# Kernel tuning notes

Hardware: AMD Instinct MI355X
Metric: run time of the kernel (lower is better)

Reference implementation:

```python
import jax, jax.numpy as jnp
import numpy as np

S = 2048   # sample_batch
N = 16     # num_h (agents per sample group)
OBS = 8
PRED = 12
H = 16     # hidden / embed size


def _lstm_cell(x, h, c, Wi, Wh, b):
    # torch LSTMCell gate order: i, f, g, o
    g = x @ Wi + h @ Wh + b
    i, f, gg, o = jnp.split(g, 4, axis=-1)
    c = jax.nn.sigmoid(f) * c + jax.nn.sigmoid(i) * jnp.tanh(gg)
    h = jax.nn.sigmoid(o) * jnp.tanh(c)
    return h, c


def setup_inputs() -> dict:
    key = jax.random.key(0)
    ks = jax.random.split(key, 16)
    B = S * N
    p = lambda k, sh: jax.random.normal(k, sh, jnp.float32) * 0.1
    return dict(
        traj_rel=jax.random.normal(ks[0], (OBS, B, 2), jnp.float32),
        obs_traj_pos=jax.random.normal(ks[1], (OBS, B, 2), jnp.float32),
        nei_index=jax.random.randint(ks[2], (B, N), 0, 2, jnp.int32),
        noise=jax.random.normal(ks[3], (PRED, B, 2), jnp.float32),
        enc_emb_W=p(ks[4], (2, H)), enc_emb_b=jnp.zeros((H,), jnp.float32),
        enc_Wi=p(ks[5], (H, 4 * H)), enc_Wh=p(ks[6], (H, 4 * H)), enc_b=jnp.zeros((4 * H,), jnp.float32),
        dec_in_W=p(ks[7], (H + 2, H)), dec_in_b=jnp.zeros((H,), jnp.float32),
        dec_Wi=p(ks[8], (H, 4 * H)), dec_Wh=p(ks[9], (H, 4 * H)), dec_b=jnp.zeros((4 * H,), jnp.float32),
        pool_rel_W=p(ks[10], (2, H)), pool_rel_b=jnp.zeros((H,), jnp.float32),
        pool_mlp_W=p(ks[11], (2 * H, H)), pool_mlp_b=jnp.zeros((H,), jnp.float32),
        out_W=p(ks[12], (H, 4)), out_b=jnp.zeros((4,), jnp.float32),
    )


def reference(traj_rel, obs_traj_pos, nei_index, noise,
              enc_emb_W, enc_emb_b, enc_Wi, enc_Wh, enc_b,
              dec_in_W, dec_in_b, dec_Wi, dec_Wh, dec_b,
              pool_rel_W, pool_rel_b, pool_mlp_W, pool_mlp_b,
              out_W, out_b):
    B = traj_rel.shape[1]
    mask = nei_index > 0  # (B, N)

    # --- history encoder: embed + LSTM over obs steps, take last hidden ---
    def enc_step(carry, x):
        h, c = carry
        e = jax.nn.relu(x @ enc_emb_W + enc_emb_b)
        h, c = _lstm_cell(e, h, c, enc_Wi, enc_Wh, enc_b)
        return (h, c), None

    h0 = jnp.zeros((B, H), traj_rel.dtype)
    (h_enc, _), _ = jax.lax.scan(enc_step, (h0, h0), traj_rel[:OBS])

    # --- neighbor pooling: embed relative pos, concat neighbor hidden, MLP, masked max-pool ---
    def pool(rel, h):
        re = jax.nn.relu(rel @ pool_rel_W + pool_rel_b)  # (B, N, H)
        hn = jnp.broadcast_to(h.reshape(S, 1, N, H), (S, N, N, H)).reshape(B, N, H)
        feat = jax.nn.relu(jnp.concatenate([re, hn], -1) @ pool_mlp_W + pool_mlp_b)
        masked = jnp.where(mask[..., None], feat, -1e9)
        pooled = masked.max(axis=1)  # (B, H)
        has = mask.any(axis=1, keepdims=True)
        return jnp.where(has, pooled, 0.0)

    def dec_step(carry, noise_t):
        h, c, ctx, out, pos = carry
        inp = jax.lax.stop_gradient(jnp.concatenate([ctx, out], -1))  # .detach() in torch
        e = jax.nn.relu(inp @ dec_in_W + dec_in_b)
        h, c = _lstm_cell(e, h, c, dec_Wi, dec_Wh, dec_b)
        p = pos.reshape(S, N, 2)
        # rel[s,i,j] = pos[s,i] - pos[s,j]  (matches expand/transpose subtraction)
        rel = (p[:, :, None, :] - p[:, None, :, :]).reshape(B, N, 2)
        ctx = pool(rel, h)
        o4 = (h + ctx) @ out_W + out_b
        mu = o4[:, :2]
        scale = jnp.clip(o4[:, 2:], -9.0, 4.0)
        std = jnp.exp(scale)
        pred = mu + std * noise_t
        pos = jax.lax.stop_gradient(pos + pred)
        return (h, c, ctx, pred, pos), (pred, mu, std)

    init = (h_enc, jnp.zeros_like(h_enc), jnp.zeros_like(h_enc),
            traj_rel[OBS - 1], obs_traj_pos[-1])
    _, (pred, mu, std) = jax.lax.scan(dec_step, init, noise)
    return pred, mu, std  # each (PRED, B, 2)
```

## Files before the change

kernel.cpp:

```cpp
#include <hip/hip_runtime.h>

#define S_    2048
#define N_    16
#define OBS_  8
#define PRED_ 12
#define B_    (S_*N_)
#define SCN_  2

typedef __attribute__((ext_vector_type(8))) short short8;
typedef __attribute__((ext_vector_type(4))) float floatx4;
typedef __attribute__((ext_vector_type(4))) unsigned uintx4;
typedef unsigned short ushort_t;

__device__ __forceinline__ float sigmf(float x) { return __builtin_amdgcn_rcpf(1.0f + __expf(-x)); }
__device__ __forceinline__ float tanhx(float x) { return fmaf(-2.0f, __builtin_amdgcn_rcpf(1.0f + __expf(2.0f*x)), 1.0f); }
__device__ __forceinline__ unsigned bfhi(float f) {
  return __builtin_bit_cast(unsigned, f) + 0x8000u;
}
__device__ __forceinline__ unsigned pack2bf(float lo, float hi) {
  return __builtin_amdgcn_perm(bfhi(hi), bfhi(lo), 0x07060302);
}
__device__ __forceinline__ ushort_t f2bf1(float f) { return (ushort_t)(bfhi(f) >> 16); }
__device__ __forceinline__ float rlanef(float v, int lane) {
  return __builtin_bit_cast(float, __builtin_amdgcn_readlane(__builtin_bit_cast(int, v), lane));
}
__device__ __forceinline__ unsigned shflu(unsigned v, int src) {
  return (unsigned)__shfl((int)v, src, 64);
}
__device__ __forceinline__ unsigned shflxu(unsigned v, int m) {
  return (unsigned)__shfl_xor((int)v, m, 64);
}

extern "C" __global__ __launch_bounds__(128, 2) void traj_ar_kernel(
    const float* __restrict__ traj_rel, const float* __restrict__ obs_pos,
    const int*  __restrict__ nei,       const float* __restrict__ noise,
    const float* __restrict__ eeW, const float* __restrict__ eeb,
    const float* __restrict__ eWi, const float* __restrict__ eWh, const float* __restrict__ eb,
    const float* __restrict__ diW, const float* __restrict__ dib,
    const float* __restrict__ dWi, const float* __restrict__ dWh, const float* __restrict__ db,
    const float* __restrict__ prW, const float* __restrict__ prb,
    const float* __restrict__ mW,  const float* __restrict__ mb,
    const float* __restrict__ oW,  const float* __restrict__ ob,
    float* __restrict__ out)
{
  __shared__ __align__(16) float h_s[SCN_][256];
  __shared__ __align__(16) float ctx_s[SCN_][256];
  __shared__ __align__(16) ushort_t ctx_bf[SCN_][384];
  __shared__            unsigned sm_s[SCN_][16];

  const int tid = threadIdx.x;
  const int w  = tid >> 6;
  const int l  = tid & 63;
  const int lq = l >> 4;
  const int lc = l & 15;
  const int u0 = lq*4;
  const int s  = blockIdx.x*SCN_ + w;
  const bool hi_half = (lq >= 2);
  const int esrc0 = (lq & 1)*32 + lc;
  const int esrc1 = esrc0 + 16;

  {
    unsigned* cz = (unsigned*)ctx_bf[w];
    cz[l] = 0; cz[64+l] = 0; cz[128+l] = 0;
  }
  float POSX = obs_pos[((OBS_-1)*B_ + s*N_ + lc)*2 + 0];
  float POSY = obs_pos[((OBS_-1)*B_ + s*N_ + lc)*2 + 1];
  unsigned prevu;
  {
    float pvx = traj_rel[((OBS_-1)*B_ + s*N_ + lc)*2 + 0];
    float pvy = traj_rel[((OBS_-1)*B_ + s*N_ + lc)*2 + 1];
    prevu = pack2bf(pvx, pvy);
  }
  {
    const int a = l >> 2, nb = (l & 3)*4;
    const int4 nv = *(const int4*)&nei[(s*N_ + a)*N_ + nb];
    unsigned bits = 0;
    bits |= (nv.x > 0) ? (1u << (nb+0)) : 0u;
    bits |= (nv.y > 0) ? (1u << (nb+1)) : 0u;
    bits |= (nv.z > 0) ? (1u << (nb+2)) : 0u;
    bits |= (nv.w > 0) ? (1u << (nb+3)) : 0u;
    bits |= __shfl_xor(bits, 1, 64);
    bits |= __shfl_xor(bits, 2, 64);
    if ((l & 3) == 0) sm_s[w][a] = bits;
  }

  short8 bfrag;
  {
    uintx4 bw;
    #pragma unroll
    for (int p = 0; p < 4; ++p)
      bw[p] = pack2bf(mW[(8*lq + 2*p)*16 + lc], mW[(8*lq + 2*p + 1)*16 + lc]);
    bfrag = __builtin_bit_cast(short8, bw);
  }
  const float bm = mb[lc];

  float pWx[8], pWy[8], pB[8];
  {
    const int wu0 = (lq & 1) * 8;
    #pragma unroll
    for (int j = 0; j < 8; ++j) {
      pWx[j] = prW[wu0 + j];
      pWy[j] = prW[16 + wu0 + j];
      pB[j]  = prb[wu0 + j];
    }
  }

  float oWc[16];
  #pragma unroll
  for (int m = 0; m < 16; ++m) oWc[m] = oW[m*4 + lq];
  const float obia = ob[lq];

  float ew0[4], ew1[4], ebv[4];
  #pragma unroll
  for (int r = 0; r < 4; ++r) {
    ew0[r] = eeW[u0+r]; ew1[r] = eeW[16+u0+r]; ebv[r] = eeb[u0+r];
  }

  const int row0 = (lq & 1) * 8;

  #define LOAD_GATE_FRAG(A, C, Wi_, Wh_, bias_, g) {                                      \
    const float* gsrc_ = (lq & 2) ? (Wh_) : (Wi_);                                        \
    uintx4 aw_;                                                                           \
    aw_[0] = pack2bf(gsrc_[(row0+0)*64 + (g)*16 + lc], gsrc_[(row0+1)*64 + (g)*16 + lc]); \
    aw_[1] = pack2bf(gsrc_[(row0+2)*64 + (g)*16 + lc], gsrc_[(row0+3)*64 + (g)*16 + lc]); \
    aw_[2] = pack2bf(gsrc_[(row0+4)*64 + (g)*16 + lc], gsrc_[(row0+5)*64 + (g)*16 + lc]); \
    aw_[3] = pack2bf(gsrc_[(row0+6)*64 + (g)*16 + lc], gsrc_[(row0+7)*64 + (g)*16 + lc]); \
    (A) = __builtin_bit_cast(short8, aw_);                                                \
    (C)[0] = (bias_)[(g)*16 + u0 + 0]; (C)[1] = (bias_)[(g)*16 + u0 + 1];                 \
    (C)[2] = (bias_)[(g)*16 + u0 + 2]; (C)[3] = (bias_)[(g)*16 + u0 + 3];                 \
  }

  short8 eA0, eA1, eA2, eA3; floatx4 eC0, eC1, eC2, eC3;
  LOAD_GATE_FRAG(eA0, eC0, eWi, eWh, eb, 0);
  LOAD_GATE_FRAG(eA1, eC1, eWi, eWh, eb, 1);
  LOAD_GATE_FRAG(eA2, eC2, eWi, eWh, eb, 2);
  LOAD_GATE_FRAG(eA3, eC3, eWi, eWh, eb, 3);

  #define LSTM_EW(r, hv) {                                                            \
    float ig = sigmf(dI[r]), fg = sigmf(dF[r]), gv = tanhx(dG[r]), og = sigmf(dO[r]); \
    c4[r] = fg*c4[r] + ig*gv;                                                         \
    hv = og * tanhx(c4[r]);                                                           \
  }

  uintx4 hf; hf[0]=0; hf[1]=0; hf[2]=0; hf[3]=0;

  floatx4 c4 = {0.0f, 0.0f, 0.0f, 0.0f};
  const float2* xr2 = (const float2*)traj_rel;
  for (int t = 0; t < OBS_; ++t) {
    float2 x = xr2[t*B_ + s*N_ + lc];
    float e0 = fmaxf(fmaf(x.y, ew1[0], fmaf(x.x, ew0[0], ebv[0])), 0.0f);
    float e1 = fmaxf(fmaf(x.y, ew1[1], fmaf(x.x, ew0[1], ebv[1])), 0.0f);
    float e2 = fmaxf(fmaf(x.y, ew1[2], fmaf(x.x, ew0[2], ebv[2])), 0.0f);
    float e3 = fmaxf(fmaf(x.y, ew1[3], fmaf(x.x, ew0[3], ebv[3])), 0.0f);
    uint2 ep; ep.x = pack2bf(e0, e1); ep.y = pack2bf(e2, e3);
    uintx4 eu;
    eu[0] = shflu(ep.x, esrc0); eu[1] = shflu(ep.y, esrc0);
    eu[2] = shflu(ep.x, esrc1); eu[3] = shflu(ep.y, esrc1);
    uintx4 bu = (lq < 2) ? eu : hf;
    short8 bfr = __builtin_bit_cast(short8, bu);
    floatx4 dI = __builtin_amdgcn_mfma_f32_16x16x32_bf16(eA0, bfr, eC0, 0, 0, 0);
    floatx4 dF = __builtin_amdgcn_mfma_f32_16x16x32_bf16(eA1, bfr, eC1, 0, 0, 0);
    floatx4 dG = __builtin_amdgcn_mfma_f32_16x16x32_bf16(eA2, bfr, eC2, 0, 0, 0);
    floatx4 dO = __builtin_amdgcn_mfma_f32_16x16x32_bf16(eA3, bfr, eC3, 0, 0, 0);
    float h40, h41, h42, h43;
    LSTM_EW(0, h40); LSTM_EW(1, h41); LSTM_EW(2, h42); LSTM_EW(3, h43);
    uint2 hp2; hp2.x = pack2bf(h40, h41); hp2.y = pack2bf(h42, h43);
    hf[0] = shflu(hp2.x, esrc0); hf[1] = shflu(hp2.y, esrc0);
    hf[2] = shflu(hp2.x, esrc1); hf[3] = shflu(hp2.y, esrc1);
  }

  short8 dA0, dA1, dA2, dA3; floatx4 dC0, dC1, dC2, dC3;
  LOAD_GATE_FRAG(dA0, dC0, dWi, dWh, db, 0);
  LOAD_GATE_FRAG(dA1, dC1, dWi, dWh, db, 1);
  LOAD_GATE_FRAG(dA2, dC2, dWi, dWh, db, 2);
  LOAD_GATE_FRAG(dA3, dC3, dWi, dWh, db, 3);

  short8 diA; floatx4 diC;
  {
    uintx4 aw; aw[0]=0; aw[1]=0; aw[2]=0; aw[3]=0;
    if (lq < 2) {
      const int r0 = lq*8;
      #pragma unroll
      for (int p = 0; p < 4; ++p)
        aw[p] = pack2bf(diW[(r0+2*p)*16 + lc], diW[(r0+2*p+1)*16 + lc]);
    } else if (lq == 2) {
      aw[0] = pack2bf(diW[16*16 + lc], diW[17*16 + lc]);
    }
    diA = __builtin_bit_cast(short8, aw);
    #pragma unroll
    for (int r = 0; r < 4; ++r) diC[r] = dib[u0 + r];
  }

  floatx4 cm[16];
  #pragma unroll
  for (int tt = 0; tt < 16; ++tt) {
    const unsigned mi = sm_s[w][tt];
    #pragma unroll
    for (int r = 0; r < 4; ++r)
      cm[tt][r] = ((mi >> (u0 + r)) & 1u) ? bm : -1e9f;
  }

  #define MK_REFRAG(pp, F0, F1) {                                           \
    const int t0_ = 2*(pp), t1_ = 2*(pp)+1;                                 \
    float rx0_ = PXs[t0_] - POSX, ry0_ = PYs[t0_] - POSY;                   \
    float rx1_ = PXs[t1_] - POSX, ry1_ = PYs[t1_] - POSY;                   \
    float rx_ = hi_half ? rx1_ : rx0_;                                      \
    float ry_ = hi_half ? ry1_ : ry0_;                                      \
    float rr_[8];                                                           \
    _Pragma("unroll")                                                       \
    for (int j = 0; j < 8; ++j)                                             \
      rr_[j] = fmaxf(fmaf(ry_, pWy[j], fmaf(rx_, pWx[j], pB[j])), 0.0f);    \
    (F0)[0] = pack2bf(rr_[0], rr_[1]);                                      \
    (F0)[1] = pack2bf(rr_[2], rr_[3]);                                      \
    (F0)[2] = pack2bf(rr_[4], rr_[5]);                                      \
    (F0)[3] = pack2bf(rr_[6], rr_[7]);                                      \
    (F1)[0] = shflxu((F0)[0], 32);                                          \
    (F1)[1] = shflxu((F0)[1], 32);                                          \
    (F1)[2] = shflxu((F0)[2], 32);                                          \
    (F1)[3] = shflxu((F0)[3], 32);                                          \
  }

  #define POOL_TILE(tt, FRAG) {                                             \
    short8 a_ = hi_half ? __builtin_bit_cast(short8, hf)                    \
                        : __builtin_bit_cast(short8, FRAG);                 \
    floatx4 d_ = __builtin_amdgcn_mfma_f32_16x16x32_bf16(a_, bfrag, cm[tt], 0, 0, 0); \
    float pm_ = fmaxf(fmaxf(d_[0], d_[1]), fmaxf(d_[2], d_[3]));            \
    pm_ = fmaxf(pm_, __shfl_xor(pm_, 16, 64));                              \
    pm_ = fmaxf(pm_, __shfl_xor(pm_, 32, 64));                              \
    if (lq == ((tt) & 3)) {                                                 \
      float cvv_ = fmaxf(pm_, 0.0f);                                        \
      ctx_s[w][(tt)*16 + lc] = cvv_;                                        \
      ctx_bf[w][(tt)*24 + lc] = f2bf1(cvv_);                                \
    }                                                                       \
  }

  c4 = (floatx4){0.0f, 0.0f, 0.0f, 0.0f};
  const int MU_OFF = PRED_*B_*2;
  const int SD_OFF = 2*PRED_*B_*2;
  for (int t = 0; t < PRED_; ++t) {
    const float nz = noise[(t*B_ + s*N_ + lc)*2 + (lq&1)];
    float PXs[16], PYs[16];
    #pragma unroll
    for (int a2 = 0; a2 < 16; ++a2) {
      PXs[a2] = rlanef(POSX, a2);
      PYs[a2] = rlanef(POSY, a2);
    }
    uintx4 g0, g1;
    MK_REFRAG(0, g0, g1);
    uint2 ep;
    {
      short8 cv = *(const short8*)&ctx_bf[w][lc*24 + (lq&1)*8];
      uintx4 pz; pz[0] = prevu; pz[1]=0; pz[2]=0; pz[3]=0;
      short8 pv = __builtin_bit_cast(short8, pz);
      short8 zz = {0,0,0,0,0,0,0,0};
      short8 bf1 = (lq < 2) ? cv : ((lq == 2) ? pv : zz);
      floatx4 d = __builtin_amdgcn_mfma_f32_16x16x32_bf16(diA, bf1, diC, 0, 0, 0);
      ep.x = pack2bf(fmaxf(d[0],0.0f), fmaxf(d[1],0.0f));
      ep.y = pack2bf(fmaxf(d[2],0.0f), fmaxf(d[3],0.0f));
    }
    {
      uintx4 eu;
      eu[0] = shflu(ep.x, esrc0); eu[1] = shflu(ep.y, esrc0);
      eu[2] = shflu(ep.x, esrc1); eu[3] = shflu(ep.y, esrc1);
      uintx4 bu = (lq < 2) ? eu : hf;
      short8 bfr = __builtin_bit_cast(short8, bu);
      floatx4 dI = __builtin_amdgcn_mfma_f32_16x16x32_bf16(dA0, bfr, dC0, 0, 0, 0);
      floatx4 dF = __builtin_amdgcn_mfma_f32_16x16x32_bf16(dA1, bfr, dC1, 0, 0, 0);
      floatx4 dG = __builtin_amdgcn_mfma_f32_16x16x32_bf16(dA2, bfr, dC2, 0, 0, 0);
      floatx4 dO = __builtin_amdgcn_mfma_f32_16x16x32_bf16(dA3, bfr, dC3, 0, 0, 0);
      float h40, h41, h42, h43;
      LSTM_EW(0, h40); LSTM_EW(1, h41); LSTM_EW(2, h42); LSTM_EW(3, h43);
      uint2 hp2; hp2.x = pack2bf(h40, h41); hp2.y = pack2bf(h42, h43);
      hf[0] = shflu(hp2.x, esrc0); hf[1] = shflu(hp2.y, esrc0);
      hf[2] = shflu(hp2.x, esrc1); hf[3] = shflu(hp2.y, esrc1);
      floatx4 hv4; hv4[0]=h40; hv4[1]=h41; hv4[2]=h42; hv4[3]=h43;
      *(floatx4*)&h_s[w][lc*16 + u0] = hv4;
    }
    {
      #pragma unroll
      for (int p = 0; p < 8; ++p) {
        uintx4 n0, n1;
        if (p < 7) MK_REFRAG(p+1, n0, n1);
        POOL_TILE(2*p,     g0);
        POOL_TILE(2*p + 1, g1);
        g0 = n0; g1 = n1;
      }
    }
    {
      float acc = obia;
      const floatx4* hp4 = (const floatx4*)&h_s[w][lc*16];
      const floatx4* cx4 = (const floatx4*)&ctx_s[w][lc*16];
      #pragma unroll
      for (int mm = 0; mm < 4; ++mm) {
        floatx4 hv = hp4[mm];
        floatx4 cv = cx4[mm];
        #pragma unroll
        for (int r = 0; r < 4; ++r)
          acc = fmaf(hv[r]+cv[r], oWc[mm*4+r], acc);
      }
      float sc = __shfl_down(acc, 32, 64);
      float mu = acc;
      float scale = fminf(fmaxf(sc, -9.0f), 4.0f);
      float sd = __expf(scale);
      float pr = fmaf(sd, nz, mu);
      if (lq < 2) {
        int o = (t*B_ + s*N_ + lc)*2 + lq;
        out[o]          = pr;
        out[MU_OFF + o] = mu;
        out[SD_OFF + o] = sd;
      }
      float prx = __shfl(pr, lc, 64);
      float pry = __shfl(pr, 16 + lc, 64);
      POSX += prx;
      POSY += pry;
      prevu = pack2bf(prx, pry);
    }
  }
  #undef LSTM_EW
  #undef LOAD_GATE_FRAG
  #undef MK_REFRAG
  #undef POOL_TILE
}

extern "C" void kernel_launch(void* const* d_in, const int* in_sizes, int n_in,
                              void* d_out, int out_size, void* d_ws, size_t ws_size,
                              hipStream_t stream) {
  (void)in_sizes; (void)n_in; (void)d_ws; (void)ws_size; (void)out_size;
  traj_ar_kernel<<<dim3(S_/SCN_), dim3(128), 0, stream>>>(
      (const float*)d_in[0],  (const float*)d_in[1],  (const int*)d_in[2],   (const float*)d_in[3],
      (const float*)d_in[4],  (const float*)d_in[5],  (const float*)d_in[6], (const float*)d_in[7],
      (const float*)d_in[8],  (const float*)d_in[9],  (const float*)d_in[10],(const float*)d_in[11],
      (const float*)d_in[12], (const float*)d_in[13], (const float*)d_in[14],(const float*)d_in[15],
      (const float*)d_in[16], (const float*)d_in[17], (const float*)d_in[18],(const float*)d_in[19],
      (float*)d_out);
}
```

Measured before the change: 160.7 us.

## Process two sample groups per wavefront with interleaved independent chains

Each wavefront now handles two sample groups (A and B) instead of one. Every phase of the encoder, decoder LSTM, pooling and output is duplicated and interleaved so that two independent dependency chains can hide MFMA and transcendental latency within a single wave. This doubles per-thread register state (two mask arrays, positions and fragments), and the launch bound drops to a minimum of 1 block per CU, which risks lower occupancy or spills. The grid halves to S/4 blocks of 128 threads.

Result: slower. 197.7 us (+23.1%).

```diff
diff --git a/kernel.cpp b/kernel.cpp
--- a/kernel.cpp
+++ b/kernel.cpp
@@ -5,7 +5,7 @@
 #define OBS_  8
 #define PRED_ 12
 #define B_    (S_*N_)
-#define SCN_  2
+#define SCN_  4
 
 typedef __attribute__((ext_vector_type(8))) short short8;
 typedef __attribute__((ext_vector_type(4))) float floatx4;
@@ -31,7 +31,7 @@
   return (unsigned)__shfl_xor((int)v, m, 64);
 }
 
-extern "C" __global__ __launch_bounds__(128, 2) void traj_ar_kernel(
+extern "C" __global__ __launch_bounds__(128, 1) void traj_ar_kernel(
     const float* __restrict__ traj_rel, const float* __restrict__ obs_pos,
     const int*  __restrict__ nei,       const float* __restrict__ noise,
     const float* __restrict__ eeW, const float* __restrict__ eeb,
@@ -54,35 +54,45 @@
   const int lq = l >> 4;
   const int lc = l & 15;
   const int u0 = lq*4;
-  const int s  = blockIdx.x*SCN_ + w;
   const bool hi_half = (lq >= 2);
+  const int slA = w*2, slB = w*2 + 1;
+  const int sA = blockIdx.x*SCN_ + slA;
+  const int sB = sA + 1;
   const int esrc0 = (lq & 1)*32 + lc;
   const int esrc1 = esrc0 + 16;
 
-  {
-    unsigned* cz = (unsigned*)ctx_bf[w];
-    cz[l] = 0; cz[64+l] = 0; cz[128+l] = 0;
-  }
-  float POSX = obs_pos[((OBS_-1)*B_ + s*N_ + lc)*2 + 0];
-  float POSY = obs_pos[((OBS_-1)*B_ + s*N_ + lc)*2 + 1];
-  unsigned prevu;
-  {
-    float pvx = traj_rel[((OBS_-1)*B_ + s*N_ + lc)*2 + 0];
-    float pvy = traj_rel[((OBS_-1)*B_ + s*N_ + lc)*2 + 1];
-    prevu = pack2bf(pvx, pvy);
-  }
-  {
-    const int a = l >> 2, nb = (l & 3)*4;
-    const int4 nv = *(const int4*)&nei[(s*N_ + a)*N_ + nb];
-    unsigned bits = 0;
-    bits |= (nv.x > 0) ? (1u << (nb+0)) : 0u;
-    bits |= (nv.y > 0) ? (1u << (nb+1)) : 0u;
-    bits |= (nv.z > 0) ? (1u << (nb+2)) : 0u;
-    bits |= (nv.w > 0) ? (1u << (nb+3)) : 0u;
-    bits |= __shfl_xor(bits, 1, 64);
-    bits |= __shfl_xor(bits, 2, 64);
-    if ((l & 3) == 0) sm_s[w][a] = bits;
-  }
+  { unsigned* cz = (unsigned*)ctx_bf[slA]; cz[l]=0; cz[64+l]=0; cz[128+l]=0; }
+  { unsigned* cz = (unsigned*)ctx_bf[slB]; cz[l]=0; cz[64+l]=0; cz[128+l]=0; }
+
+  float POSXA = obs_pos[((OBS_-1)*B_ + sA*N_ + lc)*2 + 0];
+  float POSYA = obs_pos[((OBS_-1)*B_ + sA*N_ + lc)*2 + 1];
+  float POSXB = obs_pos[((OBS_-1)*B_ + sB*N_ + lc)*2 + 0];
+  float POSYB = obs_pos[((OBS_-1)*B_ + sB*N_ + lc)*2 + 1];
+  unsigned prevuA, prevuB;
+  {
+    float px = traj_rel[((OBS_-1)*B_ + sA*N_ + lc)*2 + 0];
+    float py = traj_rel[((OBS_-1)*B_ + sA*N_ + lc)*2 + 1];
+    prevuA = pack2bf(px, py);
+  }
+  {
+    float px = traj_rel[((OBS_-1)*B_ + sB*N_ + lc)*2 + 0];
+    float py = traj_rel[((OBS_-1)*B_ + sB*N_ + lc)*2 + 1];
+    prevuB = pack2bf(px, py);
+  }
+  #define MK_MASK(sS, slS) {                                                \
+    const int a_ = l >> 2, nb_ = (l & 3)*4;                                 \
+    const int4 nv_ = *(const int4*)&nei[((sS)*N_ + a_)*N_ + nb_];           \
+    unsigned bits_ = 0;                                                     \
+    bits_ |= (nv_.x > 0) ? (1u << (nb_+0)) : 0u;                            \
+    bits_ |= (nv_.y > 0) ? (1u << (nb_+1)) : 0u;                            \
+    bits_ |= (nv_.z > 0) ? (1u << (nb_+2)) : 0u;                            \
+    bits_ |= (nv_.w > 0) ? (1u << (nb_+3)) : 0u;                            \
+    bits_ |= __shfl_xor(bits_, 1, 64);                                      \
+    bits_ |= __shfl_xor(bits_, 2, 64);                                      \
+    if ((l & 3) == 0) sm_s[slS][a_] = bits_;                                \
+  }
+  MK_MASK(sA, slA)
+  MK_MASK(sB, slB)
 
   short8 bfrag;
   {
@@ -136,37 +146,44 @@
   LOAD_GATE_FRAG(eA2, eC2, eWi, eWh, eb, 2);
   LOAD_GATE_FRAG(eA3, eC3, eWi, eWh, eb, 3);
 
-  #define LSTM_EW(r, hv) {                                                            \
+  #define LSTM_EW(C4, r, hv) {                                                        \
     float ig = sigmf(dI[r]), fg = sigmf(dF[r]), gv = tanhx(dG[r]), og = sigmf(dO[r]); \
-    c4[r] = fg*c4[r] + ig*gv;                                                         \
-    hv = og * tanhx(c4[r]);                                                           \
-  }
-
-  uintx4 hf; hf[0]=0; hf[1]=0; hf[2]=0; hf[3]=0;
-
-  floatx4 c4 = {0.0f, 0.0f, 0.0f, 0.0f};
+    (C4)[r] = fg*(C4)[r] + ig*gv;                                                     \
+    hv = og * tanhx((C4)[r]);                                                         \
+  }
+
+  #define ENC_STEP(sS, C4, HF) {                                            \
+    float2 x_ = xr2[t*B_ + (sS)*N_ + lc];                                   \
+    float e0_ = fmaxf(fmaf(x_.y, ew1[0], fmaf(x_.x, ew0[0], ebv[0])), 0.0f);\
+    float e1_ = fmaxf(fmaf(x_.y, ew1[1], fmaf(x_.x, ew0[1], ebv[1])), 0.0f);\
+    float e2_ = fmaxf(fmaf(x_.y, ew1[2], fmaf(x_.x, ew0[2], ebv[2])), 0.0f);\
+    float e3_ = fmaxf(fmaf(x_.y, ew1[3], fmaf(x_.x, ew0[3], ebv[3])), 0.0f);\
+    uint2 ep_; ep_.x = pack2bf(e0_, e1_); ep_.y = pack2bf(e2_, e3_);        \
+    uintx4 eu_;                                                             \
+    eu_[0] = shflu(ep_.x, esrc0); eu_[1] = shflu(ep_.y, esrc0);             \
+    eu_[2] = shflu(ep_.x, esrc1); eu_[3] = shflu(ep_.y, esrc1);             \
+    uintx4 bu_ = (lq < 2) ? eu_ : (HF);                                     \
+    short8 bfr_ = __builtin_bit_cast(short8, bu_);                          \
+    floatx4 dI = __builtin_amdgcn_mfma_f32_16x16x32_bf16(eA0, bfr_, eC0, 0, 0, 0); \
+    floatx4 dF = __builtin_amdgcn_mfma_f32_16x16x32_bf16(eA1, bfr_, eC1, 0, 0, 0); \
+    floatx4 dG = __builtin_amdgcn_mfma_f32_16x16x32_bf16(eA2, bfr_, eC2, 0, 0, 0); \
+    floatx4 dO = __builtin_amdgcn_mfma_f32_16x16x32_bf16(eA3, bfr_, eC3, 0, 0, 0); \
+    float h40_, h41_, h42_, h43_;                                           \
+    LSTM_EW(C4, 0, h40_); LSTM_EW(C4, 1, h41_);                             \
+    LSTM_EW(C4, 2, h42_); LSTM_EW(C4, 3, h43_);                             \
+    uint2 hp2_; hp2_.x = pack2bf(h40_, h41_); hp2_.y = pack2bf(h42_, h43_); \
+    (HF)[0] = shflu(hp2_.x, esrc0); (HF)[1] = shflu(hp2_.y, esrc0);         \
+    (HF)[2] = shflu(hp2_.x, esrc1); (HF)[3] = shflu(hp2_.y, esrc1);         \
+  }
+
+  uintx4 hfA; hfA[0]=0; hfA[1]=0; hfA[2]=0; hfA[3]=0;
+  uintx4 hfB; hfB[0]=0; hfB[1]=0; hfB[2]=0; hfB[3]=0;
+
+  floatx4 c4A = {0.0f,0.0f,0.0f,0.0f}, c4B = {0.0f,0.0f,0.0f,0.0f};
   const float2* xr2 = (const float2*)traj_rel;
   for (int t = 0; t < OBS_; ++t) {
-    float2 x = xr2[t*B_ + s*N_ + lc];
-    float e0 = fmaxf(fmaf(x.y, ew1[0], fmaf(x.x, ew0[0], ebv[0])), 0.0f);
-    float e1 = fmaxf(fmaf(x.y, ew1[1], fmaf(x.x, ew0[1], ebv[1])), 0.0f);
-    float e2 = fmaxf(fmaf(x.y, ew1[2], fmaf(x.x, ew0[2], ebv[2])), 0.0f);
-    float e3 = fmaxf(fmaf(x.y, ew1[3], fmaf(x.x, ew0[3], ebv[3])), 0.0f);
-    uint2 ep; ep.x = pack2bf(e0, e1); ep.y = pack2bf(e2, e3);
-    uintx4 eu;
-    eu[0] = shflu(ep.x, esrc0); eu[1] = shflu(ep.y, esrc0);
-    eu[2] = shflu(ep.x, esrc1); eu[3] = shflu(ep.y, esrc1);
-    uintx4 bu = (lq < 2) ? eu : hf;
-    short8 bfr = __builtin_bit_cast(short8, bu);
-    floatx4 dI = __builtin_amdgcn_mfma_f32_16x16x32_bf16(eA0, bfr, eC0, 0, 0, 0);
-    floatx4 dF = __builtin_amdgcn_mfma_f32_16x16x32_bf16(eA1, bfr, eC1, 0, 0, 0);
-    floatx4 dG = __builtin_amdgcn_mfma_f32_16x16x32_bf16(eA2, bfr, eC2, 0, 0, 0);
-    floatx4 dO = __builtin_amdgcn_mfma_f32_16x16x32_bf16(eA3, bfr, eC3, 0, 0, 0);
-    float h40, h41, h42, h43;
-    LSTM_EW(0, h40); LSTM_EW(1, h41); LSTM_EW(2, h42); LSTM_EW(3, h43);
-    uint2 hp2; hp2.x = pack2bf(h40, h41); hp2.y = pack2bf(h42, h43);
-    hf[0] = shflu(hp2.x, esrc0); hf[1] = shflu(hp2.y, esrc0);
-    hf[2] = shflu(hp2.x, esrc1); hf[3] = shflu(hp2.y, esrc1);
+    ENC_STEP(sA, c4A, hfA)
+    ENC_STEP(sB, c4B, hfB)
   }
 
   short8 dA0, dA1, dA2, dA3; floatx4 dC0, dC1, dC2, dC3;
@@ -191,25 +208,28 @@
     for (int r = 0; r < 4; ++r) diC[r] = dib[u0 + r];
   }
 
-  floatx4 cm[16];
+  floatx4 cmA[16], cmB[16];
   #pragma unroll
   for (int tt = 0; tt < 16; ++tt) {
-    const unsigned mi = sm_s[w][tt];
-    #pragma unroll
-    for (int r = 0; r < 4; ++r)
-      cm[tt][r] = ((mi >> (u0 + r)) & 1u) ? bm : -1e9f;
-  }
-
-  #define MK_REFRAG(pp, F0, F1) {                                           \
+    const unsigned miA = sm_s[slA][tt];
+    const unsigned miB = sm_s[slB][tt];
+    #pragma unroll
+    for (int r = 0; r < 4; ++r) {
+      cmA[tt][r] = ((miA >> (u0 + r)) & 1u) ? bm : -1e9f;
+      cmB[tt][r] = ((miB >> (u0 + r)) & 1u) ? bm : -1e9f;
+    }
+  }
+
+  #define MK_REFRAG(PXs, PYs, pp, PX, PY, F0, F1) {                         \
     const int t0_ = 2*(pp), t1_ = 2*(pp)+1;                                 \
-    float rx0_ = PXs[t0_] - POSX, ry0_ = PYs[t0_] - POSY;                   \
-    float rx1_ = PXs[t1_] - POSX, ry1_ = PYs[t1_] - POSY;                   \
+    float rx0_ = (PXs)[t0_] - (PX), ry0_ = (PYs)[t0_] - (PY);               \
+    float rx1_ = (PXs)[t1_] - (PX), ry1_ = (PYs)[t1_] - (PY);               \
     float rx_ = hi_half ? rx1_ : rx0_;                                      \
     float ry_ = hi_half ? ry1_ : ry0_;                                      \
     float rr_[8];                                                           \
     _Pragma("unroll")                                                       \
-    for (int j = 0; j < 8; ++j)                                             \
-      rr_[j] = fmaxf(fmaf(ry_, pWy[j], fmaf(rx_, pWx[j], pB[j])), 0.0f);    \
+    for (int j_ = 0; j_ < 8; ++j_)                                          \
+      rr_[j_] = fmaxf(fmaf(ry_, pWy[j_], fmaf(rx_, pWx[j_], pB[j_])), 0.0f);\
     (F0)[0] = pack2bf(rr_[0], rr_[1]);                                      \
     (F0)[1] = pack2bf(rr_[2], rr_[3]);                                      \
     (F0)[2] = pack2bf(rr_[4], rr_[5]);                                      \
@@ -220,106 +240,127 @@
     (F1)[3] = shflxu((F0)[3], 32);                                          \
   }
 
-  #define POOL_TILE(tt, FRAG) {                                             \
-    short8 a_ = hi_half ? __builtin_bit_cast(short8, hf)                    \
+  #define POOL_TILE(slS, CM, tt, FRAG, HF) {                                \
+    short8 a_ = hi_half ? __builtin_bit_cast(short8, HF)                    \
                         : __builtin_bit_cast(short8, FRAG);                 \
-    floatx4 d_ = __builtin_amdgcn_mfma_f32_16x16x32_bf16(a_, bfrag, cm[tt], 0, 0, 0); \
+    floatx4 d_ = __builtin_amdgcn_mfma_f32_16x16x32_bf16(a_, bfrag, (CM)[tt], 0, 0, 0); \
     float pm_ = fmaxf(fmaxf(d_[0], d_[1]), fmaxf(d_[2], d_[3]));            \
     pm_ = fmaxf(pm_, __shfl_xor(pm_, 16, 64));                              \
     pm_ = fmaxf(pm_, __shfl_xor(pm_, 32, 64));                              \
     if (lq == ((tt) & 3)) {                                                 \
       float cvv_ = fmaxf(pm_, 0.0f);                                        \
-      ctx_s[w][(tt)*16 + lc] = cvv_;                                        \
-      ctx_bf[w][(tt)*24 + lc] = f2bf1(cvv_);                                \
+      ctx_s[slS][(tt)*16 + lc] = cvv_;                                      \
+      ctx_bf[slS][(tt)*24 + lc] = f2bf1(cvv_);                              \
     }                                                                       \
   }
 
-  c4 = (floatx4){0.0f, 0.0f, 0.0f, 0.0f};
+  #define PH1(slS, PREVU, EP) {                                             \
+    short8 cv_ = *(const short8*)&ctx_bf[slS][lc*24 + (lq&1)*8];            \
+    uintx4 pz_; pz_[0] = (PREVU); pz_[1]=0; pz_[2]=0; pz_[3]=0;             \
+    short8 pv_ = __builtin_bit_cast(short8, pz_);                           \
+    short8 zz_ = {0,0,0,0,0,0,0,0};                                         \
+    short8 bf1_ = (lq < 2) ? cv_ : ((lq == 2) ? pv_ : zz_);                 \
+    floatx4 d_ = __builtin_amdgcn_mfma_f32_16x16x32_bf16(diA, bf1_, diC, 0, 0, 0); \
+    (EP).x = pack2bf(fmaxf(d_[0],0.0f), fmaxf(d_[1],0.0f));                 \
+    (EP).y = pack2bf(fmaxf(d_[2],0.0f), fmaxf(d_[3],0.0f));                 \
+  }
+
+  #define PH2(slS, EP, C4, HF) {                                            \
+    uintx4 eu_;                                                             \
+    eu_[0] = shflu((EP).x, esrc0); eu_[1] = shflu((EP).y, esrc0);           \
+    eu_[2] = shflu((EP).x, esrc1); eu_[3] = shflu((EP).y, esrc1);           \
+    uintx4 bu_ = (lq < 2) ? eu_ : (HF);                                     \
+    short8 bfr_ = __builtin_bit_cast(short8, bu_);                          \
+    floatx4 dI = __builtin_amdgcn_mfma_f32_16x16x32_bf16(dA0, bfr_, dC0, 0, 0, 0); \
+    floatx4 dF = __builtin_amdgcn_mfma_f32_16x16x32_bf16(dA1, bfr_, dC1, 0, 0, 0); \
+    floatx4 dG = __builtin_amdgcn_mfma_f32_16x16x32_bf16(dA2, bfr_, dC2, 0, 0, 0); \
+    floatx4 dO = __builtin_amdgcn_mfma_f32_16x16x32_bf16(dA3, bfr_, dC3, 0, 0, 0); \
+    float h40_, h41_, h42_, h43_;                                           \
+    LSTM_EW(C4, 0, h40_); LSTM_EW(C4, 1, h41_);                             \
+    LSTM_EW(C4, 2, h42_); LSTM_EW(C4, 3, h43_);                             \
+    uint2 hp2_; hp2_.x = pack2bf(h40_, h41_); hp2_.y = pack2bf(h42_, h43_); \
+    (HF)[0] = shflu(hp2_.x, esrc0); (HF)[1] = shflu(hp2_.y, esrc0);         \
+    (HF)[2] = shflu(hp2_.x, esrc1); (HF)[3] = shflu(hp2_.y, esrc1);         \
+    floatx4 hv4_; hv4_[0]=h40_; hv4_[1]=h41_; hv4_[2]=h42_; hv4_[3]=h43_;   \
+    *(floatx4*)&h_s[slS][lc*16 + u0] = hv4_;                                \
+  }
+
+  #define PH5(slS, sS, NZ, PX, PY, PREVU) {                                 \
+    float acc_ = obia;                                                      \
+    const floatx4* hp4_ = (const floatx4*)&h_s[slS][lc*16];                 \
+    const floatx4* cx4_ = (const floatx4*)&ctx_s[slS][lc*16];               \
+    _Pragma("unroll")                                                       \
+    for (int mm_ = 0; mm_ < 4; ++mm_) {                                     \
+      floatx4 hv_ = hp4_[mm_];                                              \
+      floatx4 cv_ = cx4_[mm_];                                              \
+      _Pragma("unroll")                                                     \
+      for (int r_ = 0; r_ < 4; ++r_)                                        \
+        acc_ = fmaf(hv_[r_]+cv_[r_], oWc[mm_*4+r_], acc_);                  \
+    }                                                                       \
+    float sc_ = __shfl_down(acc_, 32, 64);                                  \
+    float mu_ = acc_;                                                       \
+    float scale_ = fminf(fmaxf(sc_, -9.0f), 4.0f);                          \
+    float sd_ = __expf(scale_);                                             \
+    float pr_ = fmaf(sd_, (NZ), mu_);                                       \
+    if (lq < 2) {                                                           \
+      int o_ = (t*B_ + (sS)*N_ + lc)*2 + lq;                                \
+      out[o_]          = pr_;                                               \
+      out[MU_OFF + o_] = mu_;                                               \
+      out[SD_OFF + o_] = sd_;                                               \
+    }                                                                       \
+    float prx_ = __shfl(pr_, lc, 64);                                       \
+    float pry_ = __shfl(pr_, 16 + lc, 64);                                  \
+    (PX) += prx_;                                                           \
+    (PY) += pry_;                                                           \
+    (PREVU) = pack2bf(prx_, pry_);                                          \
+  }
+
+  c4A = (floatx4){0.0f,0.0f,0.0f,0.0f};
+  c4B = (floatx4){0.0f,0.0f,0.0f,0.0f};
   const int MU_OFF = PRED_*B_*2;
   const int SD_OFF = 2*PRED_*B_*2;
   for (int t = 0; t < PRED_; ++t) {
-    const float nz = noise[(t*B_ + s*N_ + lc)*2 + (lq&1)];
-    float PXs[16], PYs[16];
+    const float nzA = noise[(t*B_ + sA*N_ + lc)*2 + (lq&1)];
+    const float nzB = noise[(t*B_ + sB*N_ + lc)*2 + (lq&1)];
+    float PXsA[16], PYsA[16], PXsB[16], PYsB[16];
     #pragma unroll
     for (int a2 = 0; a2 < 16; ++a2) {
-      PXs[a2] = rlanef(POSX, a2);
-      PYs[a2] = rlanef(POSY, a2);
-    }
-    uintx4 g0, g1;
-    MK_REFRAG(0, g0, g1);
-    uint2 ep;
-    {
-      short8 cv = *(const short8*)&ctx_bf[w][lc*24 + (lq&1)*8];
-      uintx4 pz; pz[0] = prevu; pz[1]=0; pz[2]=0; pz[3]=0;
-      short8 pv = __builtin_bit_cast(short8, pz);
-      short8 zz = {0,0,0,0,0,0,0,0};
-      short8 bf1 = (lq < 2) ? cv : ((lq == 2) ? pv : zz);
-      floatx4 d = __builtin_amdgcn_mfma_f32_16x16x32_bf16(diA, bf1, diC, 0, 0, 0);
-      ep.x = pack2bf(fmaxf(d[0],0.0f), fmaxf(d[1],0.0f));
-      ep.y = pack2bf(fmaxf(d[2],0.0f), fmaxf(d[3],0.0f));
-    }
-    {
-      uintx4 eu;
-      eu[0] = shflu(ep.x, esrc0); eu[1] = shflu(ep.y, esrc0);
-      eu[2] = shflu(ep.x, esrc1); eu[3] = shflu(ep.y, esrc1);
-      uintx4 bu = (lq < 2) ? eu : hf;
-      short8 bfr = __builtin_bit_cast(short8, bu);
-      floatx4 dI = __builtin_amdgcn_mfma_f32_16x16x32_bf16(dA0, bfr, dC0, 0, 0, 0);
-      floatx4 dF = __builtin_amdgcn_mfma_f32_16x16x32_bf16(dA1, bfr, dC1, 0, 0, 0);
-      floatx4 dG = __builtin_amdgcn_mfma_f32_16x16x32_bf16(dA2, bfr, dC2, 0, 0, 0);
-      floatx4 dO = __builtin_amdgcn_mfma_f32_16x16x32_bf16(dA3, bfr, dC3, 0, 0, 0);
-      float h40, h41, h42, h43;
-      LSTM_EW(0, h40); LSTM_EW(1, h41); LSTM_EW(2, h42); LSTM_EW(3, h43);
-      uint2 hp2; hp2.x = pack2bf(h40, h41); hp2.y = pack2bf(h42, h43);
-      hf[0] = shflu(hp2.x, esrc0); hf[1] = shflu(hp2.y, esrc0);
-      hf[2] = shflu(hp2.x, esrc1); hf[3] = shflu(hp2.y, esrc1);
-      floatx4 hv4; hv4[0]=h40; hv4[1]=h41; hv4[2]=h42; hv4[3]=h43;
-      *(floatx4*)&h_s[w][lc*16 + u0] = hv4;
-    }
-    {
-      #pragma unroll
-      for (int p = 0; p < 8; ++p) {
-        uintx4 n0, n1;
-        if (p < 7) MK_REFRAG(p+1, n0, n1);
-        POOL_TILE(2*p,     g0);
-        POOL_TILE(2*p + 1, g1);
-        g0 = n0; g1 = n1;
+      PXsA[a2] = rlanef(POSXA, a2); PYsA[a2] = rlanef(POSYA, a2);
+      PXsB[a2] = rlanef(POSXB, a2); PYsB[a2] = rlanef(POSYB, a2);
+    }
+    uintx4 g0A, g1A, g0B, g1B;
+    MK_REFRAG(PXsA, PYsA, 0, POSXA, POSYA, g0A, g1A)
+    MK_REFRAG(PXsB, PYsB, 0, POSXB, POSYB, g0B, g1B)
+    uint2 epA, epB;
+    PH1(slA, prevuA, epA)
+    PH1(slB, prevuB, epB)
+    PH2(slA, epA, c4A, hfA)
+    PH2(slB, epB, c4B, hfB)
+    #pragma unroll
+    for (int p = 0; p < 8; ++p) {
+      uintx4 n0A, n1A, n0B, n1B;
+      if (p < 7) {
+        MK_REFRAG(PXsA, PYsA, p+1, POSXA, POSYA, n0A, n1A)
+        MK_REFRAG(PXsB, PYsB, p+1, POSXB, POSYB, n0B, n1B)
       }
-    }
-    {
-      float acc = obia;
-      const floatx4* hp4 = (const floatx4*)&h_s[w][lc*16];
-      const floatx4* cx4 = (const floatx4*)&ctx_s[w][lc*16];
-      #pragma unroll
-      for (int mm = 0; mm < 4; ++mm) {
-        floatx4 hv = hp4[mm];
-        floatx4 cv = cx4[mm];
-        #pragma unroll
-        for (int r = 0; r < 4; ++r)
-          acc = fmaf(hv[r]+cv[r], oWc[mm*4+r], acc);
-      }
-      float sc = __shfl_down(acc, 32, 64);
-      float mu = acc;
-      float scale = fminf(fmaxf(sc, -9.0f), 4.0f);
-      float sd = __expf(scale);
-      float pr = fmaf(sd, nz, mu);
-      if (lq < 2) {
-        int o = (t*B_ + s*N_ + lc)*2 + lq;
-        out[o]          = pr;
-        out[MU_OFF + o] = mu;
-        out[SD_OFF + o] = sd;
-      }
-      float prx = __shfl(pr, lc, 64);
-      float pry = __shfl(pr, 16 + lc, 64);
-      POSX += prx;
-      POSY += pry;
-      prevu = pack2bf(prx, pry);
-    }
+      POOL_TILE(slA, cmA, 2*p,     g0A, hfA)
+      POOL_TILE(slB, cmB, 2*p,     g0B, hfB)
+      POOL_TILE(slA, cmA, 2*p + 1, g1A, hfA)
+      POOL_TILE(slB, cmB, 2*p + 1, g1B, hfB)
+      g0A = n0A; g1A = n1A; g0B = n0B; g1B = n1B;
+    }
+    PH5(slA, sA, nzA, POSXA, POSYA, prevuA)
+    PH5(slB, sB, nzB, POSXB, POSYB, prevuB)
   }
   #undef LSTM_EW
   #undef LOAD_GATE_FRAG
   #undef MK_REFRAG
   #undef POOL_TILE
+  #undef PH1
+  #undef PH2
+  #undef PH5
+  #undef ENC_STEP
+  #undef MK_MASK
 }
 
 extern "C" void kernel_launch(void* const* d_in, const int* in_sizes, int n_in,
```
